# Kernel optimization log

Hardware: AMD Instinct MI355X
Metric: run time of the kernel (lower is better)

The kernel has to match this reference:

```python
import jax, jax.numpy as jnp
import numpy as np


def _hungarian_cols(cost):
    """Jonker-Volgenant / Hungarian (same optimum as scipy.linear_sum_assignment).
    cost: [n, n] numpy. Returns cols[i] = column assigned to row i."""
    cost = np.asarray(cost, dtype=np.float64)
    n = cost.shape[0]
    INF = np.inf
    u = np.zeros(n + 1)
    v = np.zeros(n + 1)
    p = np.zeros(n + 1, dtype=np.int64)   # p[j]: row matched to column j (1-based; 0=free)
    way = np.zeros(n + 1, dtype=np.int64)
    for i in range(1, n + 1):
        p[0] = i
        j0 = 0
        minv = np.full(n + 1, INF)
        used = np.zeros(n + 1, dtype=bool)
        while True:
            used[j0] = True
            i0 = p[j0]
            cand = cost[i0 - 1] - u[i0] - v[1:]
            free = ~used[1:]
            upd = free & (cand < minv[1:])
            minv[1:][upd] = cand[upd]
            way[1:][upd] = j0
            masked = np.where(free, minv[1:], INF)
            j1 = int(np.argmin(masked)) + 1
            delta = masked[j1 - 1]
            u[p[used]] += delta
            v[used] -= delta
            minv[~used] -= delta
            j0 = j1
            if p[j0] == 0:
                break
        while j0:
            j1 = way[j0]
            p[j0] = p[j1]
            j0 = j1
    cols = np.empty(n, dtype=np.int64)
    cols[p[1:] - 1] = np.arange(n)
    return cols


def _cdist(x, y):
    # batched euclidean distance (p=2), [B,N,D] x [B,M,D] -> [B,N,M]
    x2 = jnp.sum(x * x, axis=-1)[:, :, None]
    y2 = jnp.sum(y * y, axis=-1)[:, None, :]
    d2 = x2 + y2 - 2.0 * jnp.einsum('bnd,bmd->bnm', x, y)
    return jnp.sqrt(jnp.maximum(d2, 0.0))


def setup_inputs() -> dict:
    key = jax.random.key(0)
    k1, k2, k3 = jax.random.split(key, 3)
    B, N, D = 64, 128, 2048
    return {
        'inputs': jax.random.normal(k1, (B, N, D), dtype=jnp.float32),
        'stacked_outputs': jax.random.normal(k2, (B, N, D), dtype=jnp.float32),
        'member_probabilities': jax.random.uniform(k3, (B, N, 1), dtype=jnp.float32),
    }


def reference(inputs, stacked_outputs, member_probabilities):
    # cost matrices computed with no grad in the original (detached)
    cost = np.asarray(jax.device_get(_cdist(inputs, stacked_outputs)))
    cols = jnp.asarray(np.stack([_hungarian_cols(c) for c in cost]))  # [B, N]
    # output_mapping (match_matrix[...,None]*outputs[None,...]).sum(1) == gather rows by cols
    mapped_outputs = jnp.take_along_axis(stacked_outputs, cols[:, :, None], axis=1)
    mapped_prob = jnp.take_along_axis(member_probabilities, cols[:, :, None], axis=1)
    return mapped_outputs, mapped_prob, cols
```

## Files before the change

### kernel.cpp

```cpp
#include <hip/hip_runtime.h>

#define NB 64
#define NN 128
#define ND 2048

__global__ __launch_bounds__(256) void cost_kernel(const float* __restrict__ X,
                                                   const float* __restrict__ Y,
                                                   float* __restrict__ cost) {
  const int b  = blockIdx.x >> 2;
  const int rt = blockIdx.x & 3;
  const int rbase = rt * 32;
  __shared__ float Xs[32][33];
  __shared__ float Ys[32][129];
  __shared__ float xsq_s[32];
  __shared__ float ysq_s[128];
  const int tid = threadIdx.x;
  const int tr = tid >> 5;
  const int tc = tid & 31;
  float acc[4][4] = {{0.f,0.f,0.f,0.f},{0.f,0.f,0.f,0.f},
                     {0.f,0.f,0.f,0.f},{0.f,0.f,0.f,0.f}};
  float xsq[4] = {0.f,0.f,0.f,0.f};
  float ysq[4] = {0.f,0.f,0.f,0.f};
  const float* Xb = X + ((size_t)(b * NN + rbase)) * ND;
  const float* Yb = Y + ((size_t)(b * NN)) * ND;
  const int lrow = tid >> 3;
  const int lkk  = (tid & 7) << 2;

  for (int kb = 0; kb < ND; kb += 32) {
    __syncthreads();
    {
      float4 xv = *(const float4*)(Xb + (size_t)lrow * ND + kb + lkk);
      Xs[lkk + 0][lrow] = xv.x; Xs[lkk + 1][lrow] = xv.y;
      Xs[lkk + 2][lrow] = xv.z; Xs[lkk + 3][lrow] = xv.w;
    }
#pragma unroll
    for (int l = 0; l < 4; ++l) {
      int idx = tid + 256 * l;
      int col = idx >> 3;
      int kk  = (idx & 7) << 2;
      float4 yv = *(const float4*)(Yb + (size_t)col * ND + kb + kk);
      Ys[kk + 0][col] = yv.x; Ys[kk + 1][col] = yv.y;
      Ys[kk + 2][col] = yv.z; Ys[kk + 3][col] = yv.w;
    }
    __syncthreads();
#pragma unroll 4
    for (int kk = 0; kk < 32; ++kk) {
      float xv[4], yv[4];
#pragma unroll
      for (int ii = 0; ii < 4; ++ii) xv[ii] = Xs[kk][4 * tr + ii];
#pragma unroll
      for (int jj = 0; jj < 4; ++jj) yv[jj] = Ys[kk][tc + 32 * jj];
#pragma unroll
      for (int ii = 0; ii < 4; ++ii) xsq[ii] += xv[ii] * xv[ii];
#pragma unroll
      for (int jj = 0; jj < 4; ++jj) ysq[jj] += yv[jj] * yv[jj];
#pragma unroll
      for (int ii = 0; ii < 4; ++ii)
#pragma unroll
        for (int jj = 0; jj < 4; ++jj)
          acc[ii][jj] += xv[ii] * yv[jj];
    }
  }
  if (tc == 0) {
#pragma unroll
    for (int ii = 0; ii < 4; ++ii) xsq_s[4 * tr + ii] = xsq[ii];
  }
  if (tr == 0) {
#pragma unroll
    for (int jj = 0; jj < 4; ++jj) ysq_s[tc + 32 * jj] = ysq[jj];
  }
  __syncthreads();
#pragma unroll
  for (int ii = 0; ii < 4; ++ii) {
    int r = rbase + 4 * tr + ii;
    float xs = xsq_s[4 * tr + ii];
#pragma unroll
    for (int jj = 0; jj < 4; ++jj) {
      int c = tc + 32 * jj;
      float d2 = xs + ysq_s[c] - 2.0f * acc[ii][jj];
      cost[((size_t)(b * NN + r)) * NN + c] = sqrtf(fmaxf(d2, 0.0f));
    }
  }
}

__device__ __forceinline__ unsigned umin2(unsigned a, unsigned b) { return a < b ? a : b; }

__device__ __forceinline__ unsigned wave_min_u32(unsigned x) {
  unsigned t;
  t = (unsigned)__builtin_amdgcn_update_dpp((int)x, (int)x, 0x111, 0xF, 0xF, false); x = umin2(x, t);
  t = (unsigned)__builtin_amdgcn_update_dpp((int)x, (int)x, 0x112, 0xF, 0xF, false); x = umin2(x, t);
  t = (unsigned)__builtin_amdgcn_update_dpp((int)x, (int)x, 0x114, 0xF, 0xF, false); x = umin2(x, t);
  t = (unsigned)__builtin_amdgcn_update_dpp((int)x, (int)x, 0x118, 0xF, 0xF, false); x = umin2(x, t);
  t = (unsigned)__builtin_amdgcn_update_dpp((int)x, (int)x, 0x142, 0xA, 0xF, false); x = umin2(x, t);
  t = (unsigned)__builtin_amdgcn_update_dpp((int)x, (int)x, 0x143, 0xC, 0xF, false); x = umin2(x, t);
  return (unsigned)__builtin_amdgcn_readlane((int)x, 63);
}

__device__ __forceinline__ double readlane_f64(double d, int lane) {
  int lo = __builtin_amdgcn_readlane(__double2loint(d), lane);
  int hi = __builtin_amdgcn_readlane(__double2hiint(d), lane);
  return __hiloint2double(hi, lo);
}

__global__ __launch_bounds__(64) void hungarian_kernel(const float* __restrict__ cost,
                                                       int* __restrict__ cols) {
  const int b = blockIdx.x;
  const int lane = threadIdx.x;
  __shared__ float cst[NN * NN];
  __shared__ int colrow[NN];
  __shared__ int rwin[NN];
  __shared__ double u_row[NN + 1];
  __shared__ int queue[4 * NN + 8];
  __shared__ int qcnt[1];

  {
    const float4* src = (const float4*)(cost + (size_t)b * NN * NN);
    float4* dst = (float4*)cst;
    for (int t = lane; t < NN * NN / 4; t += 64) dst[t] = src[t];
  }
  for (int t = lane; t <= NN; t += 64) u_row[t] = 0.0;
  __syncthreads();

  float cmin[2]; int cargr[2];
#pragma unroll
  for (int k2 = 0; k2 < 2; ++k2) {
    const int j = lane + 64 * k2;
    float mn = cst[j]; int ar = 0;
    for (int r = 1; r < NN; ++r) {
      float cr = cst[r * NN + j];
      if (cr < mn) { mn = cr; ar = r; }
    }
    cmin[k2] = mn; cargr[k2] = ar;
    colrow[j] = ar;
  }
  __syncthreads();
  int rowwin[2] = {-1, -1};
  for (int j = 0; j < NN; ++j) {
    int rr = colrow[j];
#pragma unroll
    for (int k2 = 0; k2 < 2; ++k2) {
      if (rr == lane + 64 * k2 && rowwin[k2] < 0) rowwin[k2] = j;
    }
  }
#pragma unroll
  for (int k2 = 0; k2 < 2; ++k2) rwin[lane + 64 * k2] = rowwin[k2];
  const unsigned long long mask0 = __ballot(rowwin[0] >= 0);
  const unsigned long long mask1 = __ballot(rowwin[1] >= 0);
  __syncthreads();

  int    p_[2];
  double pu_[2], v_[2];
#pragma unroll
  for (int k2 = 0; k2 < 2; ++k2) {
    const int j = lane + 64 * k2;
    const int r = cargr[k2];
    p_[k2]  = (rwin[r] == j) ? (r + 1) : 0;
    pu_[k2] = 0.0;
    v_[k2]  = (double)cmin[k2];
  }

  if (lane == 0) {
    int t = 0;
    for (int r = 1; r <= NN; ++r) {
      const bool m = (r - 1) < 64 ? ((mask0 >> (r - 1)) & 1ull)
                                  : ((mask1 >> (r - 65)) & 1ull);
      if (!m) queue[t++] = r;
    }
    qcnt[0] = t;
  }
  __syncthreads();
  {
    int head = 0, tail = qcnt[0];
    for (int pops = 0; head < tail && pops < 3 * NN; ++pops) {
      const int i = queue[head++];
      const float* crow = cst + (i - 1) * NN;
      const double d0 = (double)crow[lane]      - v_[0];
      const double d1 = (double)crow[lane + 64] - v_[1];
      double m1, m2; int j1;
      if (d1 < d0) { m1 = d1; j1 = lane + 64; m2 = d0; }
      else         { m1 = d0; j1 = lane;      m2 = d1; }
#pragma unroll
      for (int off = 32; off > 0; off >>= 1) {
        const double om1 = __shfl_xor(m1, off);
        const double om2 = __shfl_xor(m2, off);
        const int    oj1 = __shfl_xor(j1, off);
        const double nm2 = fmin(fmin(m2, om2), fmax(m1, om1));
        const bool take = (om1 < m1) || (om1 == m1 && oj1 < j1);
        if (take) { m1 = om1; j1 = oj1; }
        m2 = nm2;
      }
      const int own = j1 & 63, hk = j1 >> 6;
      const int    psel  = hk ? p_[1]  : p_[0];
      const double pusel = hk ? pu_[1] : pu_[0];
      const int k = __builtin_amdgcn_readlane(psel, own);
      const double oldpu = readlane_f64(pusel, own);
      if (lane == own) {
        if (hk) { v_[1] -= (m2 - m1); p_[1] = i; pu_[1] = m2; }
        else    { v_[0] -= (m2 - m1); p_[0] = i; pu_[0] = m2; }
      }
      if (lane == 0) {
        u_row[i] = m2;
        if (k != 0) { u_row[k] = oldpu; queue[tail] = k; }
      }
      if (k != 0) ++tail;
      __syncthreads();
    }
  }
  __syncthreads();

  for (int t = lane; t < NN; t += 64) colrow[t] = 0;
  __syncthreads();
  if (p_[0] > 0) colrow[p_[0] - 1] = 1;
  if (p_[1] > 0) colrow[p_[1] - 1] = 1;
  __syncthreads();
  const unsigned long long fmask0 = __ballot(colrow[lane] == 0);
  const unsigned long long fmask1 = __ballot(colrow[lane + 64] == 0);

  const unsigned INFBITS = 0x7f800000u;

  for (int i = 1; i <= NN; ++i) {
    const bool freerow = (i - 1) < 64 ? ((fmask0 >> (i - 1)) & 1ull)
                                      : ((fmask1 >> (i - 65)) & 1ull);
    if (!freerow) continue;

    const double u_i = u_row[i];
    double D_[2]; int way_[2]; int used_[2] = {0, 0};
    {
      const float* crow = &cst[(i - 1) * NN];
      D_[0] = (double)crow[lane]      - u_i - v_[0];  way_[0] = 0;
      D_[1] = (double)crow[lane + 64] - u_i - v_[1];  way_[1] = 0;
    }
    double Dfinal = 0.0; int jF = 1;
    for (int it = 0; it < NN + 2; ++it) {
      const float pr0 = used_[0] ? __uint_as_float(INFBITS) : fmaxf((float)D_[0], 0.0f);
      const float pr1 = used_[1] ? __uint_as_float(INFBITS) : fmaxf((float)D_[1], 0.0f);
      const int   k2l = (pr1 < pr0) ? 1 : 0;
      const unsigned key = __float_as_uint(k2l ? pr1 : pr0);
      const unsigned rmin = wave_min_u32(key);
      const unsigned long long wm = __ballot(key == rmin);
      const int winlane = (int)__ffsll(wm) - 1;
      const int    psel = k2l ? p_[1]  : p_[0];
      const double Dsel = k2l ? D_[1]  : D_[0];
      const double usel = k2l ? pu_[1] : pu_[0];
      const int i0 = __builtin_amdgcn_readlane(psel, winlane);
      const double bv = readlane_f64(Dsel, winlane);
      const int k2w = __builtin_amdgcn_readlane(k2l, winlane);
      const int bj = 1 + winlane + (k2w << 6);
      if (i0 == 0) { Dfinal = bv; jF = bj; break; }
      const float* crow = &cst[(i0 - 1) * NN];
      const float c0 = crow[lane];
      const float c1 = crow[lane + 64];
      const double u0 = readlane_f64(usel, winlane);
      if (lane == winlane) { if (k2w) used_[1] = 1; else used_[0] = 1; }
      const double base = bv - u0;
      if (!used_[0]) {
        const double cand = (double)c0 + base - v_[0];
        if (cand < D_[0]) { D_[0] = cand; way_[0] = bj; }
      }
      if (!used_[1]) {
        const double cand = (double)c1 + base - v_[1];
        if (cand < D_[1]) { D_[1] = cand; way_[1] = bj; }
      }
    }
#pragma unroll
    for (int k2 = 0; k2 < 2; ++k2) {
      if (used_[k2]) {
        const double diff = Dfinal - D_[k2];
        v_[k2]  -= diff;
        pu_[k2] += diff;
      }
    }
    int j = jF;
    for (int g = 0; g < NN + 2; ++g) {
      const int own = (j - 1) & 63;
      const int hk  = (j - 1) >> 6;
      const int wsel = hk ? way_[1] : way_[0];
      const int wj = __builtin_amdgcn_readlane(wsel, own);
      int pn; double pun;
      if (wj == 0) { pn = i; pun = u_i + Dfinal; }
      else {
        const int o2 = (wj - 1) & 63, h2 = (wj - 1) >> 6;
        const int    psel2  = h2 ? p_[1]  : p_[0];
        const double pusel2 = h2 ? pu_[1] : pu_[0];
        pn  = __builtin_amdgcn_readlane(psel2, o2);
        pun = readlane_f64(pusel2, o2);
      }
      if (lane == own) {
        if (hk) { p_[1] = pn; pu_[1] = pun; }
        else    { p_[0] = pn; pu_[0] = pun; }
      }
      if (wj == 0) break;
      j = wj;
    }
  }

#pragma unroll
  for (int k2 = 0; k2 < 2; ++k2) {
    const int r = p_[k2] - 1;
    if (r >= 0 && r < NN) cols[b * NN + r] = lane + 64 * k2;
  }
}

__global__ __launch_bounds__(256) void gather_kernel(const float* __restrict__ outs,
                                                     const float* __restrict__ probs,
                                                     const int* __restrict__ cols,
                                                     float* __restrict__ out) {
  const int bi = blockIdx.x;
  const int b  = bi >> 7;
  const int col = cols[bi] & (NN - 1);
  const float4* src = (const float4*)(outs + ((size_t)(b * NN + col)) * ND);
  float4* dst = (float4*)(out + (size_t)bi * ND);
  const int t = threadIdx.x;
  dst[t]       = src[t];
  dst[t + 256] = src[t + 256];
  if (t == 0) {
    const size_t PROB_OFF = (size_t)NB * NN * ND;
    out[PROB_OFF + bi]        = probs[b * NN + col];
    out[PROB_OFF + 8192 + bi] = (float)(cols[bi] & (NN - 1));
  }
}

extern "C" void kernel_launch(void* const* d_in, const int* in_sizes, int n_in,
                              void* d_out, int out_size, void* d_ws, size_t ws_size,
                              hipStream_t stream) {
  const float* X = (const float*)d_in[0];
  const float* Y = (const float*)d_in[1];
  const float* P = (const float*)d_in[2];
  float* out = (float*)d_out;

  float* cost = (float*)d_ws;
  int* cols = (int*)((char*)d_ws + (size_t)NB * NN * NN * 4);

  cost_kernel<<<dim3(NB * 4), dim3(256), 0, stream>>>(X, Y, cost);
  hungarian_kernel<<<dim3(NB), dim3(64), 0, stream>>>(cost, cols);
  gather_kernel<<<dim3(NB * NN), dim3(256), 0, stream>>>(Y, P, cols, out);
}
```

Baseline: 834.8 us.

## Add matched-row dual reduction, DPP top-two min in auction, packed readlane in augment

Adds a reduction-transfer pass: for each initially matched row, the second-smallest reduced cost is computed and subtracted from the matched column's dual, which tightens the duals before augmentation. The auction phase replaces the shuffle-based double top-two reduction with a DPP-based 32-bit float-key top-two min, then uses ballots and readlanes to recover the exact double values. The augmenting-path loop packs the row index and half selector into one readlane and issues the cost-row load before the exit branch, so the LDS latency overlaps the readlanes. The new pass costs 128 serial wave reductions, and keying on floats can pick a different element on near-ties.

After: 696.1 us. 16.6% less time.

```diff
diff --git a/kernel.cpp b/kernel.cpp
--- a/kernel.cpp
+++ b/kernel.cpp
@@ -84,6 +84,7 @@
 }
 
 __device__ __forceinline__ unsigned umin2(unsigned a, unsigned b) { return a < b ? a : b; }
+__device__ __forceinline__ unsigned umax2(unsigned a, unsigned b) { return a > b ? a : b; }
 
 __device__ __forceinline__ unsigned wave_min_u32(unsigned x) {
   unsigned t;
@@ -94,6 +95,27 @@
   t = (unsigned)__builtin_amdgcn_update_dpp((int)x, (int)x, 0x142, 0xA, 0xF, false); x = umin2(x, t);
   t = (unsigned)__builtin_amdgcn_update_dpp((int)x, (int)x, 0x143, 0xC, 0xF, false); x = umin2(x, t);
   return (unsigned)__builtin_amdgcn_readlane((int)x, 63);
+}
+
+template <int CTRL, int RMASK>
+__device__ __forceinline__ void min2_step(unsigned& a, unsigned& b) {
+  unsigned ap = (unsigned)__builtin_amdgcn_update_dpp((int)a, (int)a, CTRL, RMASK, 0xF, false);
+  unsigned bp = (unsigned)__builtin_amdgcn_update_dpp((int)b, (int)b, CTRL, RMASK, 0xF, false);
+  unsigned hi = umax2(a, ap);
+  a = umin2(a, ap);
+  b = umin2(umin2(b, bp), hi);
+}
+
+__device__ __forceinline__ void wave_min2_u32(unsigned a, unsigned b,
+                                              unsigned& m1k, unsigned& m2k) {
+  min2_step<0x111, 0xF>(a, b);
+  min2_step<0x112, 0xF>(a, b);
+  min2_step<0x114, 0xF>(a, b);
+  min2_step<0x118, 0xF>(a, b);
+  min2_step<0x142, 0xA>(a, b);
+  min2_step<0x143, 0xC>(a, b);
+  m1k = (unsigned)__builtin_amdgcn_readlane((int)a, 63);
+  m2k = (unsigned)__builtin_amdgcn_readlane((int)b, 63);
 }
 
 __device__ __forceinline__ double readlane_f64(double d, int lane) {
@@ -159,6 +181,27 @@
     v_[k2]  = (double)cmin[k2];
   }
 
+  for (int i = 1; i <= NN; ++i) {
+    const bool matched = (i - 1) < 64 ? ((mask0 >> (i - 1)) & 1ull)
+                                      : ((mask1 >> (i - 65)) & 1ull);
+    if (!matched) continue;
+    const int j1 = rwin[i - 1];
+    const float* crow = &cst[(i - 1) * NN];
+    double d0 = (double)crow[lane]      - v_[0];
+    double d1 = (double)crow[lane + 64] - v_[1];
+    if (lane == (j1 & 63)) { if (j1 >> 6) d1 = 1e300; else d0 = 1e300; }
+    const double dmn = fmin(d0, d1);
+    const unsigned k = __float_as_uint((float)dmn);
+    const unsigned mk = wave_min_u32(k);
+    const unsigned long long bm = __ballot(k == mk);
+    const int wl = (int)__ffsll(bm) - 1;
+    const double mu = readlane_f64(dmn, wl);
+    if (lane == (j1 & 63)) {
+      if (j1 >> 6) { v_[1] -= mu; pu_[1] = mu; }
+      else         { v_[0] -= mu; pu_[0] = mu; }
+    }
+  }
+
   if (lane == 0) {
     int t = 0;
     for (int r = 1; r <= NN; ++r) {
@@ -176,23 +219,28 @@
       const float* crow = cst + (i - 1) * NN;
       const double d0 = (double)crow[lane]      - v_[0];
       const double d1 = (double)crow[lane + 64] - v_[1];
-      double m1, m2; int j1;
-      if (d1 < d0) { m1 = d1; j1 = lane + 64; m2 = d0; }
-      else         { m1 = d0; j1 = lane;      m2 = d1; }
-#pragma unroll
-      for (int off = 32; off > 0; off >>= 1) {
-        const double om1 = __shfl_xor(m1, off);
-        const double om2 = __shfl_xor(m2, off);
-        const int    oj1 = __shfl_xor(j1, off);
-        const double nm2 = fmin(fmin(m2, om2), fmax(m1, om1));
-        const bool take = (om1 < m1) || (om1 == m1 && oj1 < j1);
-        if (take) { m1 = om1; j1 = oj1; }
-        m2 = nm2;
-      }
+      double dmn, dmx; int jmn;
+      if (d1 < d0) { dmn = d1; dmx = d0; jmn = lane + 64; }
+      else         { dmn = d0; dmx = d1; jmn = lane; }
+      const unsigned ka = __float_as_uint((float)dmn);
+      const unsigned kb = __float_as_uint((float)dmx);
+      unsigned m1k, m2k;
+      wave_min2_u32(ka, kb, m1k, m2k);
+      const unsigned long long bA = __ballot(ka == m1k);
+      const int win = (int)__ffsll(bA) - 1;
+      const double m1 = readlane_f64(dmn, win);
+      const int j1 = __builtin_amdgcn_readlane(jmn, win);
+      const unsigned long long bA2 = __ballot(ka == m2k) & ~(1ull << win);
+      const unsigned long long bB2 = __ballot(kb == m2k);
+      const int lA = bA2 ? (int)__ffsll(bA2) - 1 : 64;
+      const int lB = bB2 ? (int)__ffsll(bB2) - 1 : 64;
+      double m2 = (lA <= lB) ? readlane_f64(dmn, lA < 64 ? lA : 63)
+                             : readlane_f64(dmx, lB < 64 ? lB : 63);
+      m2 = fmax(m2, m1);
       const int own = j1 & 63, hk = j1 >> 6;
       const int    psel  = hk ? p_[1]  : p_[0];
       const double pusel = hk ? pu_[1] : pu_[0];
-      const int k = __builtin_amdgcn_readlane(psel, own);
+      const int kk = __builtin_amdgcn_readlane(psel, own);
       const double oldpu = readlane_f64(pusel, own);
       if (lane == own) {
         if (hk) { v_[1] -= (m2 - m1); p_[1] = i; pu_[1] = m2; }
@@ -200,9 +248,9 @@
       }
       if (lane == 0) {
         u_row[i] = m2;
-        if (k != 0) { u_row[k] = oldpu; queue[tail] = k; }
-      }
-      if (k != 0) ++tail;
+        if (kk != 0) { u_row[kk] = oldpu; queue[tail] = kk; }
+      }
+      if (kk != 0) ++tail;
       __syncthreads();
     }
   }
@@ -239,18 +287,17 @@
       const unsigned rmin = wave_min_u32(key);
       const unsigned long long wm = __ballot(key == rmin);
       const int winlane = (int)__ffsll(wm) - 1;
-      const int    psel = k2l ? p_[1]  : p_[0];
-      const double Dsel = k2l ? D_[1]  : D_[0];
-      const double usel = k2l ? pu_[1] : pu_[0];
-      const int i0 = __builtin_amdgcn_readlane(psel, winlane);
-      const double bv = readlane_f64(Dsel, winlane);
-      const int k2w = __builtin_amdgcn_readlane(k2l, winlane);
+      const int metal = ((k2l ? p_[1] : p_[0]) << 1) | k2l;
+      const int meta = __builtin_amdgcn_readlane(metal, winlane);
+      const int i0 = meta >> 1;
+      const int k2w = meta & 1;
       const int bj = 1 + winlane + (k2w << 6);
-      if (i0 == 0) { Dfinal = bv; jF = bj; break; }
-      const float* crow = &cst[(i0 - 1) * NN];
+      const float* crow = &cst[((i0 - 1) & 127) * NN];
       const float c0 = crow[lane];
       const float c1 = crow[lane + 64];
-      const double u0 = readlane_f64(usel, winlane);
+      const double bv = readlane_f64(k2l ? D_[1] : D_[0], winlane);
+      if (i0 == 0) { Dfinal = bv; jF = bj; break; }
+      const double u0 = readlane_f64(k2l ? pu_[1] : pu_[0], winlane);
       if (lane == winlane) { if (k2w) used_[1] = 1; else used_[0] = 1; }
       const double base = bv - u0;
       if (!used_[0]) {
```
